# Kernel optimization log

Hardware: AMD Instinct MI355X
Metric: run time of the kernel (lower is better)

Reference implementation:

```python
import jax, jax.numpy as jnp
import numpy as np

# BiDiGemma (Aveygo/SRNext) wrapping RecurrentGemma-style ResidualBlocks:
#   block0 = RECURRENT (causal conv width 4 + RG-LRU linear recurrence)
#   block1 = local (sliding-window, MQA) ATTENTION with partial RoPE
# Dropout(0.1) is treated as eval-mode identity.

B, S, D, H = 4, 4096, 256, 4
HD = D // H            # head dim = 64
E = 3 * D              # mlp_expanded_width = expand_ratio * dim
W_ATT = D              # attention_window_size = dim = 256 (divides S)
TW = 4                 # recurrentgemma temporal conv width
_NEG = -2.3819763e38   # recurrentgemma masking constant

_PNAMES = ["ln_gamma","ln_beta","proj_w","proj_b","fconv_w","fconv_b","bconv_w","bconv_b",
 "rn0_t","rn0_c","ly_w","ly_b","lx_w","lx_b","lo_w","lo_b","c1d_w","c1d_b",
 "a_param","ig_w","ig_b","ag_w","ag_b","mlp0_up_w","mlp0_up_b","mlp0_dn_w","mlp0_dn_b",
 "rn1_t","rn1_c","q_w","k_w","v_w","o_w","o_b","mlp1_up_w","mlp1_up_b","mlp1_dn_w","mlp1_dn_b"]


def _init_params(key):
    ks = iter(jax.random.split(key, 24))
    nrm = lambda shape, s: jax.random.normal(next(ks), shape, jnp.float32) * s
    p = {}
    p["ln_gamma"] = jnp.ones((D,), jnp.float32); p["ln_beta"] = jnp.zeros((D,), jnp.float32)
    p["proj_w"] = nrm((D, D), D ** -0.5);  p["proj_b"] = jnp.zeros((D,), jnp.float32)
    p["fconv_w"] = nrm((D, D), D ** -0.5); p["fconv_b"] = jnp.zeros((D,), jnp.float32)
    p["bconv_w"] = nrm((D, D), D ** -0.5); p["bconv_b"] = jnp.zeros((D,), jnp.float32)
    p["rn0_t"] = jnp.zeros((D,), jnp.float32); p["rn0_c"] = jnp.zeros((D,), jnp.float32)
    p["ly_w"] = nrm((D, D), D ** -0.5); p["ly_b"] = jnp.zeros((D,), jnp.float32)
    p["lx_w"] = nrm((D, D), D ** -0.5); p["lx_b"] = jnp.zeros((D,), jnp.float32)
    p["lo_w"] = nrm((D, D), D ** -0.5); p["lo_b"] = jnp.zeros((D,), jnp.float32)
    p["c1d_w"] = nrm((TW, D), 0.1);     p["c1d_b"] = jnp.zeros((D,), jnp.float32)
    p["a_param"] = jnp.log(jnp.expm1(jnp.linspace(0.9, 1.5, D, dtype=jnp.float32)))
    p["ig_w"] = nrm((H, HD, HD), HD ** -0.5); p["ig_b"] = jnp.zeros((H, HD), jnp.float32)
    p["ag_w"] = nrm((H, HD, HD), HD ** -0.5); p["ag_b"] = jnp.zeros((H, HD), jnp.float32)
    p["mlp0_up_w"] = nrm((2, D, E), D ** -0.5); p["mlp0_up_b"] = jnp.zeros((2, E), jnp.float32)
    p["mlp0_dn_w"] = nrm((E, D), E ** -0.5);    p["mlp0_dn_b"] = jnp.zeros((D,), jnp.float32)
    p["rn1_t"] = jnp.zeros((D,), jnp.float32); p["rn1_c"] = jnp.zeros((D,), jnp.float32)
    p["q_w"] = nrm((D, D), D ** -0.5); p["k_w"] = nrm((D, HD), D ** -0.5); p["v_w"] = nrm((D, HD), D ** -0.5)
    p["o_w"] = nrm((D, D), D ** -0.5); p["o_b"] = jnp.zeros((D,), jnp.float32)
    p["mlp1_up_w"] = nrm((2, D, E), D ** -0.5); p["mlp1_up_b"] = jnp.zeros((2, E), jnp.float32)
    p["mlp1_dn_w"] = nrm((E, D), E ** -0.5);    p["mlp1_dn_b"] = jnp.zeros((D,), jnp.float32)
    return p


def _gelu(x):
    return jax.nn.gelu(x, approximate=False)  # torch F.gelu default (erf)


def _rms_norm(x, scale, eps=1e-6):
    var = jnp.mean(jnp.square(x), axis=-1, keepdims=True)
    return x * jax.lax.rsqrt(var + eps) * (1.0 + scale)


def _layer_norm(x, g, b, eps=1e-5):
    m = jnp.mean(x, axis=-1, keepdims=True)
    v = jnp.mean(jnp.square(x - m), axis=-1, keepdims=True)
    return (x - m) * jax.lax.rsqrt(v + eps) * g + b


def _block_diag(x, w, b):
    # BlockDiagonalLinear: per-head [HD x HD] blocks
    xh = x.reshape(*x.shape[:-1], H, HD)
    y = jnp.einsum('bshd,hdk->bshk', xh, w) + b
    return y.reshape(*x.shape)


def _causal_conv1d(x, w, b):
    # depthwise causal conv, w: [TW, D], w[TW-1] multiplies current token
    xp = jnp.pad(x, ((0, 0), (TW - 1, 0), (0, 0)))
    out = sum(xp[:, i:i + x.shape[1], :] * w[i] for i in range(TW))
    return out + b


def _rg_lru(x, pos, a_param, ig_w, ig_b, ag_w, ag_b):
    gate_x = jax.nn.sigmoid(_block_diag(x, ig_w, ig_b))
    gate_a = jax.nn.sigmoid(_block_diag(x, ag_w, ag_b))
    log_a = -8.0 * gate_a * jax.nn.softplus(a_param)   # c = 8
    a = jnp.exp(log_a)
    mult = jnp.sqrt(-jnp.expm1(2.0 * log_a))           # sqrt(1 - a^2)
    reset = (pos == 0)[..., None]
    mult = jnp.where(reset, 1.0, mult)
    bterm = x * gate_x * mult
    def comb(e1, e2):
        a1, b1 = e1
        a2, b2 = e2
        return a1 * a2, a2 * b1 + b2
    _, h = jax.lax.associative_scan(comb, (a, bterm), axis=1)
    return h


def _rope(x, pos):
    # partial RoPE: applied to first half of head dim (recurrentgemma)
    rot, rest = jnp.split(x, 2, axis=-1)
    f = rot.shape[-1] // 2
    inv_freq = 10000.0 ** (-(2.0 / rot.shape[-1]) * jnp.arange(f, dtype=jnp.float32))
    t = pos[..., None, None].astype(jnp.float32) * inv_freq  # [b, s, 1, f]
    sin, cos = jnp.sin(t), jnp.cos(t)
    x1, x2 = jnp.split(rot, 2, axis=-1)
    return jnp.concatenate([x1 * cos - x2 * sin, x2 * cos + x1 * sin, rest], axis=-1)


def _local_attention(x, pos, q_w, k_w, v_w, o_w, o_b):
    # MQA sliding-window attention, window = W_ATT; chunked to honor locality
    b, s, _ = x.shape
    q = (x @ q_w).reshape(b, s, H, HD)
    k = (x @ k_w).reshape(b, s, 1, HD)
    v = (x @ v_w).reshape(b, s, HD)
    q = _rope(q, pos) * (HD ** -0.5)
    k = _rope(k, pos)[:, :, 0]
    Wn = W_ATT
    nb = s // Wn
    qc = q.reshape(b, nb, Wn, H, HD)
    kp = jnp.pad(k, ((0, 0), (Wn, 0), (0, 0))).reshape(b, nb + 1, Wn, HD)
    vp = jnp.pad(v, ((0, 0), (Wn, 0), (0, 0))).reshape(b, nb + 1, Wn, HD)
    kc = jnp.concatenate([kp[:, :-1], kp[:, 1:]], axis=2)  # [b, nb, 2W, HD]
    vc = jnp.concatenate([vp[:, :-1], vp[:, 1:]], axis=2)
    logits = jnp.einsum('bnqhd,bnkd->bnhqk', qc, kc)
    i = jnp.arange(Wn)[:, None]
    j = jnp.arange(2 * Wn)[None, :]
    diff = (i + Wn) - j                       # q_pos - k_pos
    base = (diff >= 0) & (diff <= Wn)         # causal & q <= k + window_size
    cidx = jnp.arange(nb)[:, None, None]
    mask = base[None] & ((cidx > 0) | (j[None] >= Wn))  # no left padding in chunk 0
    logits = jnp.where(mask[None, :, None], logits, _NEG)
    probs = jax.nn.softmax(logits, axis=-1)
    out = jnp.einsum('bnhqk,bnkd->bnqhd', probs, vc).reshape(b, s, D)
    return out @ o_w + o_b


def _mlp(x, up_w, up_b, dn_w, dn_b):
    up = jnp.einsum('bsd,cde->cbse', x, up_w) + up_b[:, None, None, :]
    act = _gelu(up[0]) * up[1]
    return act @ dn_w + dn_b


def _gemma_block(x, pos, p):
    # ResidualBlock 0: RECURRENT
    raw = x
    xn = _rms_norm(raw, p['rn0_t'])
    y = _gelu(xn @ p['ly_w'] + p['ly_b'])
    xr = xn @ p['lx_w'] + p['lx_b']
    xr = _causal_conv1d(xr, p['c1d_w'], p['c1d_b'])
    xr = _rg_lru(xr, pos, p['a_param'], p['ig_w'], p['ig_b'], p['ag_w'], p['ag_b'])
    xr = (xr * y) @ p['lo_w'] + p['lo_b']
    residual = xr + raw
    x = _rms_norm(residual, p['rn0_c'])
    x = _mlp(x, p['mlp0_up_w'], p['mlp0_up_b'], p['mlp0_dn_w'], p['mlp0_dn_b']) + residual
    # ResidualBlock 1: local ATTENTION
    raw = x
    xn = _rms_norm(raw, p['rn1_t'])
    xa = _local_attention(xn, pos, p['q_w'], p['k_w'], p['v_w'], p['o_w'], p['o_b'])
    residual = xa + raw
    x = _rms_norm(residual, p['rn1_c'])
    x = _mlp(x, p['mlp1_up_w'], p['mlp1_up_b'], p['mlp1_dn_w'], p['mlp1_dn_b']) + residual
    return x


def _forward(skip, *params):
    p = dict(zip(_PNAMES, params))
    b, s, _ = skip.shape
    pos = jnp.broadcast_to(jnp.arange(s, dtype=jnp.int32)[None], (b, s))
    x = _layer_norm(skip, p['ln_gamma'], p['ln_beta']) @ p['proj_w'] + p['proj_b']
    z = jax.nn.sigmoid(jnp.mean(jax.nn.silu(skip), axis=-1, keepdims=True))
    fwd = _gemma_block(x @ p['fconv_w'] + p['fconv_b'], pos, p)  # Conv1d k=1 == pointwise
    bwd = _gemma_block(x @ p['bconv_w'] + p['bconv_b'], pos, p)
    return z * (fwd + bwd) + skip


def setup_inputs() -> dict:
    key = jax.random.key(0)
    kx, kp = jax.random.split(key)
    inp = {"skip": jax.random.normal(kx, (B, S, D), jnp.float32)}
    inp.update(_init_params(kp))
    return inp


def reference(skip, ln_gamma, ln_beta, proj_w, proj_b, fconv_w, fconv_b, bconv_w, bconv_b, rn0_t, rn0_c, ly_w, ly_b, lx_w, lx_b, lo_w, lo_b, c1d_w, c1d_b, a_param, ig_w, ig_b, ag_w, ag_b, mlp0_up_w, mlp0_up_b, mlp0_dn_w, mlp0_dn_b, rn1_t, rn1_c, q_w, k_w, v_w, o_w, o_b, mlp1_up_w, mlp1_up_b, mlp1_dn_w, mlp1_dn_b):
    return _forward(skip, ln_gamma, ln_beta, proj_w, proj_b, fconv_w, fconv_b, bconv_w, bconv_b, rn0_t, rn0_c, ly_w, ly_b, lx_w, lx_b, lo_w, lo_b, c1d_w, c1d_b, a_param, ig_w, ig_b, ag_w, ag_b, mlp0_up_w, mlp0_up_b, mlp0_dn_w, mlp0_dn_b, rn1_t, rn1_c, q_w, k_w, v_w, o_w, o_b, mlp1_up_w, mlp1_up_b, mlp1_dn_w, mlp1_dn_b)
```

## Files before the change

kernel.cpp:

```cpp
#include <hip/hip_runtime.h>
#include <math.h>
#include <stddef.h>


#define BB   4
#define SS   4096
#define DD   256
#define HH   4
#define HDIM 64
#define EE   768
#define RR   (BB*SS)
#define RR2  (2*RR)
#define WNN  256
#define CH   64
#define NCH  (SS/CH)

typedef __attribute__((ext_vector_type(8))) short bfrag;
typedef __attribute__((ext_vector_type(4))) float f4acc;

__device__ __forceinline__ float geluf(float x){
  float u = 1.5957691216f*(x + 0.044715f*x*x*x);
  float e = __expf(u);
  float t = 1.f - 2.f/(e+1.f);
  return 0.5f*x*(1.f+t);
}
__device__ __forceinline__ float sigm(float x){ return 1.0f/(1.0f+expf(-x)); }

__device__ __forceinline__ unsigned short f2bf(float x){
  unsigned u = __float_as_uint(x);
  return (unsigned short)((u + 0x7FFFu + ((u>>16)&1u)) >> 16);
}
__device__ __forceinline__ float bf2f(unsigned short h){
  return __uint_as_float(((unsigned)h) << 16);
}
__device__ __forceinline__ void split2(float v, unsigned short* h, unsigned short* l){
  unsigned short hb = f2bf(v);
  *h = hb; *l = f2bf(v - bf2f(hb));
}

__device__ __forceinline__ float wredSum(float v){
#pragma unroll
  for(int o=32;o>0;o>>=1) v += __shfl_xor(v,o,64);
  return v;
}

__global__ __launch_bounds__(256) void ln_z_k(const float* __restrict__ skip,
    const float* __restrict__ g, const float* __restrict__ b,
    unsigned short* __restrict__ oh, unsigned short* __restrict__ ol,
    float* __restrict__ z)
{
  int row  = blockIdx.x*4 + (threadIdx.x>>6);
  int lane = threadIdx.x & 63;
  float4 v = ((const float4*)(skip + (size_t)row*DD))[lane];
  float s  = v.x+v.y+v.z+v.w;
  float sq = v.x*v.x+v.y*v.y+v.z*v.z+v.w*v.w;
  float si = v.x*sigm(v.x)+v.y*sigm(v.y)+v.z*sigm(v.z)+v.w*sigm(v.w);
  s = wredSum(s); sq = wredSum(sq); si = wredSum(si);
  float mean = s*(1.0f/DD);
  float var  = sq*(1.0f/DD) - mean*mean;
  float inv  = rsqrtf(var + 1e-5f);
  float4 gv = ((const float4*)g)[lane];
  float4 bv = ((const float4*)b)[lane];
  float o0 = (v.x-mean)*inv*gv.x + bv.x;
  float o1 = (v.y-mean)*inv*gv.y + bv.y;
  float o2 = (v.z-mean)*inv*gv.z + bv.z;
  float o3 = (v.w-mean)*inv*gv.w + bv.w;
  ushort4 hi, lo;
  split2(o0,&hi.x,&lo.x); split2(o1,&hi.y,&lo.y);
  split2(o2,&hi.z,&lo.z); split2(o3,&hi.w,&lo.w);
  ((ushort4*)(oh + (size_t)row*DD))[lane] = hi;
  ((ushort4*)(ol + (size_t)row*DD))[lane] = lo;
  if(lane==0) z[row] = sigm(si*(1.0f/DD));
}

__global__ __launch_bounds__(256) void rms_k(const float* __restrict__ x,
    const float* __restrict__ t,
    unsigned short* __restrict__ oh, unsigned short* __restrict__ ol)
{
  int row  = blockIdx.x*4 + (threadIdx.x>>6);
  int lane = threadIdx.x & 63;
  float4 v = ((const float4*)(x + (size_t)row*DD))[lane];
  float sq = v.x*v.x+v.y*v.y+v.z*v.z+v.w*v.w;
  sq = wredSum(sq);
  float inv = rsqrtf(sq*(1.0f/DD) + 1e-6f);
  float4 tv = ((const float4*)t)[lane];
  float o0 = v.x*inv*(1.0f+tv.x);
  float o1 = v.y*inv*(1.0f+tv.y);
  float o2 = v.z*inv*(1.0f+tv.z);
  float o3 = v.w*inv*(1.0f+tv.w);
  ushort4 hi, lo;
  split2(o0,&hi.x,&lo.x); split2(o1,&hi.y,&lo.y);
  split2(o2,&hi.z,&lo.z); split2(o3,&hi.w,&lo.w);
  ((ushort4*)(oh + (size_t)row*DD))[lane] = hi;
  ((ushort4*)(ol + (size_t)row*DD))[lane] = lo;
}

struct TS  { const float* s; unsigned short* h; unsigned short* l; int K; int N; };
struct TS8 { TS t[8]; };

__global__ __launch_bounds__(256) void tsplit8_k(TS8 g){
  TS tt = g.t[blockIdx.y];
  int idx = blockIdx.x*256 + threadIdx.x;
  int tot = tt.K*tt.N;
  if(idx >= tot) return;
  int k = idx / tt.N;
  int n = idx - k*tt.N;
  float x = tt.s[idx];
  unsigned short hb = f2bf(x);
  unsigned short lb = f2bf(x - bf2f(hb));
  tt.h[(size_t)n*tt.K + k] = hb;
  tt.l[(size_t)n*tt.K + k] = lb;
}

template<int BN, int MODE, int DUAL, int OUT, int TERMS>
__global__ __launch_bounds__(256) void gemm_mfma(
    const unsigned short* __restrict__ Ah_g, const unsigned short* __restrict__ Al_g,
    const unsigned short* __restrict__ B0h, const unsigned short* __restrict__ B0l,
    const unsigned short* __restrict__ B1h, const unsigned short* __restrict__ B1l,
    const float* __restrict__ bias0, const float* __restrict__ bias1,
    const float* __restrict__ Res, float* __restrict__ C,
    unsigned short* __restrict__ Ch, unsigned short* __restrict__ Cl,
    int K, int lda, int ldc)
{
  constexpr int NT = BN/32;
  constexpr int ST = 40;
  __shared__ unsigned short Ash[128*ST];
  __shared__ unsigned short Asl[TERMS==3 ? 128*ST : 8];
  __shared__ unsigned short Bsh[BN*ST];
  __shared__ unsigned short Bsl[TERMS>=2 ? BN*ST : 8];
  __shared__ unsigned short B2h[DUAL?BN*ST:8];
  __shared__ unsigned short B2l[(DUAL && TERMS>=2)?BN*ST:8];

  const int tid  = threadIdx.x;
  const int lane = tid & 63, wave = tid >> 6;
  const int wm = wave >> 1, wn = wave & 1;
  const int bm = blockIdx.y*128, bn = blockIdx.x*BN;
  const int m16 = lane & 15, q = lane >> 4;

  f4acc acc[4][NT];
  f4acc acc2[DUAL?4:1][DUAL?NT:1];
#pragma unroll
  for(int i=0;i<4;i++)
#pragma unroll
    for(int j=0;j<NT;j++){
      acc[i][j] = (f4acc)0.f;
      if constexpr(DUAL) acc2[i][j] = (f4acc)0.f;
    }

  const int r0 = tid >> 2, c0 = tid & 3;
  const int coff = c0*8;
  const int d0 = r0*ST + coff, d1 = (r0+64)*ST + coff;

  const unsigned short* pAh0 = Ah_g + (size_t)(bm+r0)*lda + coff;
  const unsigned short* pAh1 = pAh0 + (size_t)64*lda;
  const unsigned short* pAl0 = (TERMS==3) ? (Al_g + (size_t)(bm+r0)*lda + coff)
                                          : (const unsigned short*)nullptr;
  const unsigned short* pAl1 = (TERMS==3) ? (pAl0 + (size_t)64*lda)
                                          : (const unsigned short*)nullptr;
  const unsigned short *pB0h0=nullptr,*pB0h1=nullptr,*pB0l0=nullptr,*pB0l1=nullptr;
  const unsigned short *pBa=nullptr,*pBb=nullptr,*pBc=nullptr,*pBd=nullptr;
  if constexpr(BN==128){
    pB0h0 = B0h + (size_t)(bn+r0)*K + coff;  pB0h1 = pB0h0 + (size_t)64*K;
    if constexpr(TERMS>=2){
      pB0l0 = B0l + (size_t)(bn+r0)*K + coff;  pB0l1 = pB0l0 + (size_t)64*K;
    }
  } else {
    pBa = B0h + (size_t)(bn+r0)*K + coff;
    if constexpr(TERMS>=2) pBb = B0l + (size_t)(bn+r0)*K + coff;
    if constexpr(DUAL){
      pBc = B1h + (size_t)(bn+r0)*K + coff;
      if constexpr(TERMS>=2) pBd = B1l + (size_t)(bn+r0)*K + coff;
    }
  }

  for(int k0 = 0; k0 < K; k0 += 32){
    *(float4*)&Ash[d0] = *(const float4*)(pAh0 + k0);
    *(float4*)&Ash[d1] = *(const float4*)(pAh1 + k0);
    if constexpr(TERMS==3){
      *(float4*)&Asl[d0] = *(const float4*)(pAl0 + k0);
      *(float4*)&Asl[d1] = *(const float4*)(pAl1 + k0);
    }
    if constexpr(BN==128){
      *(float4*)&Bsh[d0] = *(const float4*)(pB0h0 + k0);
      *(float4*)&Bsh[d1] = *(const float4*)(pB0h1 + k0);
      if constexpr(TERMS>=2){
        *(float4*)&Bsl[d0] = *(const float4*)(pB0l0 + k0);
        *(float4*)&Bsl[d1] = *(const float4*)(pB0l1 + k0);
      }
    } else {
      *(float4*)&Bsh[d0] = *(const float4*)(pBa + k0);
      if constexpr(TERMS>=2) *(float4*)&Bsl[d0] = *(const float4*)(pBb + k0);
      if constexpr(DUAL){
        *(float4*)&B2h[d0] = *(const float4*)(pBc + k0);
        if constexpr(TERMS>=2) *(float4*)&B2l[d0] = *(const float4*)(pBd + k0);
      }
    }
    __syncthreads();

    bfrag ah[4], al[TERMS==3?4:1], b0hf[NT], b0lf[TERMS>=2?NT:1];
    bfrag b1hf[DUAL?NT:1], b1lf[(DUAL&&TERMS>=2)?NT:1];
#pragma unroll
    for(int mi=0;mi<4;mi++){
      int row = wm*64 + mi*16 + m16;
      ah[mi] = *(const bfrag*)&Ash[row*ST + q*8];
      if constexpr(TERMS==3) al[mi] = *(const bfrag*)&Asl[row*ST + q*8];
    }
#pragma unroll
    for(int ni=0;ni<NT;ni++){
      int n = wn*(BN/2) + ni*16 + m16;
      b0hf[ni] = *(const bfrag*)&Bsh[n*ST + q*8];
      if constexpr(TERMS>=2) b0lf[ni] = *(const bfrag*)&Bsl[n*ST + q*8];
      if constexpr(DUAL){
        b1hf[ni] = *(const bfrag*)&B2h[n*ST + q*8];
        if constexpr(TERMS>=2) b1lf[ni] = *(const bfrag*)&B2l[n*ST + q*8];
      }
    }
#pragma unroll
    for(int mi=0;mi<4;mi++)
#pragma unroll
      for(int ni=0;ni<NT;ni++){
        acc[mi][ni] = __builtin_amdgcn_mfma_f32_16x16x32_bf16(ah[mi], b0hf[ni], acc[mi][ni],0,0,0);
        if constexpr(TERMS>=2)
          acc[mi][ni] = __builtin_amdgcn_mfma_f32_16x16x32_bf16(ah[mi], b0lf[ni], acc[mi][ni],0,0,0);
        if constexpr(TERMS==3)
          acc[mi][ni] = __builtin_amdgcn_mfma_f32_16x16x32_bf16(al[mi], b0hf[ni], acc[mi][ni],0,0,0);
        if constexpr(DUAL){
          acc2[mi][ni] = __builtin_amdgcn_mfma_f32_16x16x32_bf16(ah[mi], b1hf[ni], acc2[mi][ni],0,0,0);
          if constexpr(TERMS>=2)
            acc2[mi][ni] = __builtin_amdgcn_mfma_f32_16x16x32_bf16(ah[mi], b1lf[ni], acc2[mi][ni],0,0,0);
          if constexpr(TERMS==3)
            acc2[mi][ni] = __builtin_amdgcn_mfma_f32_16x16x32_bf16(al[mi], b1hf[ni], acc2[mi][ni],0,0,0);
        }
      }
    __syncthreads();
  }

  if constexpr(OUT==0 || OUT==1 || OUT==5){
#pragma unroll
    for(int ni=0;ni<NT;ni++){
      const int col = bn + wn*(BN/2) + ni*16 + m16;
      float bv0 = (MODE&1) ? bias0[col] : 0.f;
      float bv1 = DUAL ? bias1[col] : 0.f;
#pragma unroll
      for(int mi=0;mi<4;mi++){
#pragma unroll
        for(int r=0;r<4;r++){
          const int row = bm + wm*64 + mi*16 + q*4 + r;
          float v = acc[mi][ni][r] + bv0;
          if constexpr(DUAL){
            float v2 = acc2[mi][ni][r] + bv1;
            v = geluf(v) * v2;
          } else if(MODE&2){
            v = geluf(v);
          }
          if(MODE&8) v += Res[(size_t)row*ldc + col];
          if constexpr(OUT==0){
            C[(size_t)row*ldc + col] = v;
          } else if constexpr(OUT==1){
            unsigned short hb = f2bf(v);
            Ch[(size_t)row*ldc + col] = hb;
            Cl[(size_t)row*ldc + col] = f2bf(v - bf2f(hb));
          } else {
            Ch[(size_t)row*ldc + col] = f2bf(v);
          }
        }
      }
    }
  } else if constexpr(OUT==2){
    const int hb = bn + wn*64;
    const float p = (float)m16;
    const float invf = __expf(-p * 0.575646273248511f);
#pragma unroll
    for(int mi=0;mi<4;mi++){
#pragma unroll
      for(int r=0;r<4;r++){
        const int row = bm + wm*64 + mi*16 + q*4 + r;
        const int s = row & (SS-1);
        float t = (float)s * invf;
        float sn, cs; __sincosf(t, &sn, &cs);
        float x1 = acc[mi][0][r], x2 = acc[mi][1][r];
        float v0 = (x1*cs - x2*sn)*0.125f;
        float v1 = (x2*cs + x1*sn)*0.125f;
        float v2 = acc[mi][2][r]*0.125f;
        float v3 = acc[mi][3][r]*0.125f;
        size_t base = (size_t)row*ldc + hb;
        unsigned short hh;
        hh=f2bf(v0); Ch[base+m16]=hh;    Cl[base+m16]   =f2bf(v0-bf2f(hh));
        hh=f2bf(v1); Ch[base+16+m16]=hh; Cl[base+16+m16]=f2bf(v1-bf2f(hh));
        hh=f2bf(v2); Ch[base+32+m16]=hh; Cl[base+32+m16]=f2bf(v2-bf2f(hh));
        hh=f2bf(v3); Ch[base+48+m16]=hh; Cl[base+48+m16]=f2bf(v3-bf2f(hh));
      }
    }
  } else if constexpr(OUT==3){
    const float p = (float)m16;
    const float invf = __expf(-p * 0.575646273248511f);
#pragma unroll
    for(int mi=0;mi<4;mi++){
#pragma unroll
      for(int r=0;r<4;r++){
        const int row = bm + wm*64 + mi*16 + q*4 + r;
        const int s = row & (SS-1);
        float v0, v1;
        if(wn==0){
          float t = (float)s * invf;
          float sn, cs; __sincosf(t, &sn, &cs);
          float x1 = acc[mi][0][r], x2 = acc[mi][1][r];
          v0 = x1*cs - x2*sn;
          v1 = x2*cs + x1*sn;
        } else {
          v0 = acc[mi][0][r]; v1 = acc[mi][1][r];
        }
        size_t base = (size_t)row*ldc + wn*32;
        unsigned short hh;
        hh=f2bf(v0); Ch[base+m16]=hh;    Cl[base+m16]   =f2bf(v0-bf2f(hh));
        hh=f2bf(v1); Ch[base+16+m16]=hh; Cl[base+16+m16]=f2bf(v1-bf2f(hh));
      }
    }
  } else if constexpr(OUT==4){
#pragma unroll
    for(int ni=0;ni<NT;ni++){
      const int col = wn*32 + ni*16 + m16;
#pragma unroll
      for(int mi=0;mi<4;mi++){
        const int rowb = bm + wm*64 + mi*16 + q*4;
        const int b = rowb >> 12, sl = rowb & (SS-1);
        ushort4 hv;
        hv.x = f2bf(acc[mi][ni][0]); hv.y = f2bf(acc[mi][ni][1]);
        hv.z = f2bf(acc[mi][ni][2]); hv.w = f2bf(acc[mi][ni][3]);
        *(ushort4*)(Ch + ((size_t)(b*64 + col))*SS + sl) = hv;
      }
    }
  }
}

__global__ __launch_bounds__(256) void conv_split_k(const float* __restrict__ x,
    const float* __restrict__ w, const float* __restrict__ b,
    unsigned short* __restrict__ oh, unsigned short* __restrict__ ol)
{
  int idx = blockIdx.x*256 + threadIdx.x;
  int d = idx & (DD-1);
  int r = idx >> 8;
  int s = r & (SS-1);
  float acc = b[d];
#pragma unroll
  for(int i=0;i<4;i++){
    int t = s - 3 + i;
    if(t >= 0) acc += w[i*DD + d] * x[(size_t)(r-3+i)*DD + d];
  }
  unsigned short hb = f2bf(acc);
  oh[idx] = hb;
  ol[idx] = f2bf(acc - bf2f(hb));
}

__global__ __launch_bounds__(256) void gates_mfma_k(
    const unsigned short* __restrict__ Xh, const unsigned short* __restrict__ Xl,
    const unsigned short* __restrict__ igth, const unsigned short* __restrict__ igtl,
    const unsigned short* __restrict__ agth, const unsigned short* __restrict__ agtl,
    const float* __restrict__ igb, const float* __restrict__ agb,
    const float* __restrict__ ap,
    float* __restrict__ Aout, float* __restrict__ Bout)
{
  constexpr int ST = 72;
  __shared__ unsigned short Ash[128*ST];
  __shared__ unsigned short Asl[128*ST];

  const int h  = blockIdx.x;
  const int bm = blockIdx.y*128;
  const int tid = threadIdx.x;
  const int lane = tid & 63, wave = tid >> 6;
  const int wm = wave >> 1, wn = wave & 1;
  const int m16 = lane & 15, q = lane >> 4;

  {
    const int r = tid >> 1, kq = (tid & 1)*32;
    const size_t src = (size_t)(bm + r)*DD + h*HDIM + kq;
    const int dst = r*ST + kq;
#pragma unroll
    for(int i=0;i<4;i++){
      *(float4*)&Ash[dst + i*8] = *(const float4*)(Xh + src + i*8);
      *(float4*)&Asl[dst + i*8] = *(const float4*)(Xl + src + i*8);
    }
  }
  __syncthreads();

  f4acc accI[4][2], accA[4][2];
#pragma unroll
  for(int i=0;i<4;i++)
#pragma unroll
    for(int j=0;j<2;j++){ accI[i][j]=(f4acc)0.f; accA[i][j]=(f4acc)0.f; }

  const size_t wbase = (size_t)h*HDIM*HDIM;
#pragma unroll
  for(int ks=0;ks<2;ks++){
    bfrag ah[4], al[4];
#pragma unroll
    for(int mi=0;mi<4;mi++){
      const int row = wm*64 + mi*16 + m16;
      ah[mi] = *(const bfrag*)&Ash[row*ST + ks*32 + q*8];
      al[mi] = *(const bfrag*)&Asl[row*ST + ks*32 + q*8];
    }
#pragma unroll
    for(int ni=0;ni<2;ni++){
      const size_t bo = wbase + (size_t)(wn*32 + ni*16 + m16)*HDIM + ks*32 + q*8;
      bfrag bIh = *(const bfrag*)(igth + bo);
      bfrag bIl = *(const bfrag*)(igtl + bo);
      bfrag bAh = *(const bfrag*)(agth + bo);
      bfrag bAl = *(const bfrag*)(agtl + bo);
#pragma unroll
      for(int mi=0;mi<4;mi++){
        accI[mi][ni] = __builtin_amdgcn_mfma_f32_16x16x32_bf16(ah[mi], bIh, accI[mi][ni],0,0,0);
        accI[mi][ni] = __builtin_amdgcn_mfma_f32_16x16x32_bf16(ah[mi], bIl, accI[mi][ni],0,0,0);
        accI[mi][ni] = __builtin_amdgcn_mfma_f32_16x16x32_bf16(al[mi], bIh, accI[mi][ni],0,0,0);
        accA[mi][ni] = __builtin_amdgcn_mfma_f32_16x16x32_bf16(ah[mi], bAh, accA[mi][ni],0,0,0);
        accA[mi][ni] = __builtin_amdgcn_mfma_f32_16x16x32_bf16(ah[mi], bAl, accA[mi][ni],0,0,0);
        accA[mi][ni] = __builtin_amdgcn_mfma_f32_16x16x32_bf16(al[mi], bAh, accA[mi][ni],0,0,0);
      }
    }
  }

#pragma unroll
  for(int ni=0;ni<2;ni++){
    const int cl  = wn*32 + ni*16 + m16;
    const int col = h*HDIM + cl;
    const float bI = igb[col], bA = agb[col];
    const float apv = ap[col];
    const float sp = (apv > 20.f) ? apv : log1pf(expf(apv));
#pragma unroll
    for(int mi=0;mi<4;mi++){
#pragma unroll
      for(int r=0;r<4;r++){
        const int lrow = wm*64 + mi*16 + q*4 + r;
        const int row = bm + lrow;
        const int s = row & (SS-1);
        float gx = 1.f/(1.f + __expf(-(accI[mi][ni][r] + bI)));
        float ga = 1.f/(1.f + __expf(-(accA[mi][ni][r] + bA)));
        float la = -8.f * ga * sp;
        float a_ = __expf(la);
        float mult = (s==0) ? 1.f : sqrtf(fmaxf(1.f - __expf(2.f*la), 0.f));
        float x = bf2f(Ash[lrow*ST + cl]) + bf2f(Asl[lrow*ST + cl]);
        Aout[(size_t)row*DD + col] = a_;
        Bout[(size_t)row*DD + col] = x * gx * mult;
      }
    }
  }
}

__global__ __launch_bounds__(256) void scan1_k(const float* __restrict__ A,
    const float* __restrict__ Bv, float* __restrict__ csa, float* __restrict__ csb)
{
  int idx = blockIdx.x*256 + threadIdx.x;
  int d = idx & (DD-1);
  int c = (idx >> 8) & (NCH-1);
  int b = idx >> 14;
  size_t base = ((size_t)b*SS + (size_t)c*CH)*DD + d;
  float Aa = 1.f, Bb_ = 0.f;
  for(int t=0;t<CH;t++){
    float a  = A [base + (size_t)t*DD];
    float bb = Bv[base + (size_t)t*DD];
    Aa  = a*Aa;
    Bb_ = a*Bb_ + bb;
  }
  csa[idx] = Aa; csb[idx] = Bb_;
}

__global__ __launch_bounds__(256) void scan2_k(const float* __restrict__ csa,
    float* __restrict__ csb)
{
  int idx = blockIdx.x*256 + threadIdx.x;
  int d = idx & (DD-1);
  int b = idx >> 8;
  float h = 0.f;
  for(int c=0;c<NCH;c++){
    size_t i = ((size_t)b*NCH + c)*DD + d;
    float Aa = csa[i], Bb_ = csb[i];
    csb[i] = h;
    h = Aa*h + Bb_;
  }
}

__global__ __launch_bounds__(256) void scan3_k(const float* __restrict__ A,
    const float* __restrict__ Bv, const float* __restrict__ csb,
    const unsigned short* __restrict__ Yh,
    unsigned short* __restrict__ Hh, unsigned short* __restrict__ Hl)
{
  int idx = blockIdx.x*256 + threadIdx.x;
  int d = idx & (DD-1);
  int c = (idx >> 8) & (NCH-1);
  int b = idx >> 14;
  size_t base = ((size_t)b*SS + (size_t)c*CH)*DD + d;
  float h = csb[idx];
  for(int t=0;t<CH;t++){
    float a  = A [base + (size_t)t*DD];
    float bb = Bv[base + (size_t)t*DD];
    h = a*h + bb;
    float v = h * bf2f(Yh[base + (size_t)t*DD]);
    unsigned short hb = f2bf(v);
    Hh[base + (size_t)t*DD] = hb;
    Hl[base + (size_t)t*DD] = f2bf(v - bf2f(hb));
  }
}

#define AST 72
__global__ __launch_bounds__(256) void attn_k(
    const unsigned short* __restrict__ Qh, const unsigned short* __restrict__ Ql,
    const unsigned short* __restrict__ Kh, const unsigned short* __restrict__ Kl,
    const unsigned short* __restrict__ Vt,
    unsigned short* __restrict__ Oh, unsigned short* __restrict__ Ol)
{
  __shared__ unsigned short Ksh[64*AST], Ksl[64*AST], Vsh[64*AST];
  __shared__ unsigned short Ps[4*16*AST];

  const int qt = blockIdx.x & 3, n = blockIdx.x >> 2;
  const int h = blockIdx.y, b = blockIdx.z;
  const int tid = threadIdx.x;
  const int lane = tid & 63, w = tid >> 6;
  const int m16 = lane & 15, q = lane >> 4;
  const int s0 = n*WNN + qt*64;

  const size_t qro = ((size_t)(b*SS + s0 + w*16 + m16))*DD + h*HDIM + q*8;
  bfrag qh0 = *(const bfrag*)(Qh + qro);
  bfrag qh1 = *(const bfrag*)(Qh + qro + 32);
  bfrag ql0 = *(const bfrag*)(Ql + qro);
  bfrag ql1 = *(const bfrag*)(Ql + qro + 32);

  float mrow[4], lrow[4];
  f4acc oacc[4];
#pragma unroll
  for(int i=0;i<4;i++){ mrow[i]=-3.0e38f; lrow[i]=0.f; oacc[i]=(f4acc)0.f; }

  const int ktlo = (n==0) ? 4 : qt;
  const int kthi = qt + 4;
  const int sr = tid >> 2, sc = tid & 3;

  for(int kt=ktlo; kt<=kthi; kt++){
    const int kbase = (n-1)*WNN + kt*64;
#pragma unroll
    for(int cc=0; cc<2; cc++){
      int g = sc + cc*4;
      *(float4*)&Ksh[sr*AST + g*8] =
        *(const float4*)(Kh + (size_t)(b*SS + kbase + sr)*HDIM + g*8);
      *(float4*)&Ksl[sr*AST + g*8] =
        *(const float4*)(Kl + (size_t)(b*SS + kbase + sr)*HDIM + g*8);
      *(float4*)&Vsh[sr*AST + g*8] =
        *(const float4*)(Vt + ((size_t)(b*64 + sr))*SS + kbase + g*8);
    }
    __syncthreads();

    f4acc sacc[4];
#pragma unroll
    for(int nt=0;nt<4;nt++) sacc[nt] = (f4acc)0.f;
#pragma unroll
    for(int nt=0;nt<4;nt++){
      const int kr = (nt*16+m16)*AST;
      bfrag kh0 = *(const bfrag*)&Ksh[kr + q*8];
      bfrag kh1 = *(const bfrag*)&Ksh[kr + 32 + q*8];
      bfrag kl0 = *(const bfrag*)&Ksl[kr + q*8];
      bfrag kl1 = *(const bfrag*)&Ksl[kr + 32 + q*8];
      sacc[nt] = __builtin_amdgcn_mfma_f32_16x16x32_bf16(qh0, kh0, sacc[nt],0,0,0);
      sacc[nt] = __builtin_amdgcn_mfma_f32_16x16x32_bf16(qh0, kl0, sacc[nt],0,0,0);
      sacc[nt] = __builtin_amdgcn_mfma_f32_16x16x32_bf16(ql0, kh0, sacc[nt],0,0,0);
      sacc[nt] = __builtin_amdgcn_mfma_f32_16x16x32_bf16(qh1, kh1, sacc[nt],0,0,0);
      sacc[nt] = __builtin_amdgcn_mfma_f32_16x16x32_bf16(qh1, kl1, sacc[nt],0,0,0);
      sacc[nt] = __builtin_amdgcn_mfma_f32_16x16x32_bf16(ql1, kh1, sacc[nt],0,0,0);
    }

    const bool needlo = (kt == qt+4);
    const bool needhi = (kt == qt);
#pragma unroll
    for(int r=0;r<4;r++){
      int qp = qt*64 + w*16 + q*4 + r;
      float sv[4];
      float tm = -3.0e38f;
#pragma unroll
      for(int nt=0;nt<4;nt++){
        float scv = sacc[nt][r];
        if(needlo || needhi){
          int kj = kt*64 + nt*16 + m16;
          int diff = qp + WNN - kj;
          bool ok = (!needlo || diff >= 0) && (!needhi || diff <= WNN);
          scv = ok ? scv : -3.0e38f;
        }
        sv[nt] = scv;
        tm = fmaxf(tm, scv);
      }
#pragma unroll
      for(int off=1; off<16; off<<=1) tm = fmaxf(tm, __shfl_xor(tm, off, 64));
      float mn = fmaxf(mrow[r], tm);
      float alpha = __expf(mrow[r]-mn);
      float rs = 0.f;
#pragma unroll
      for(int nt=0;nt<4;nt++){
        float pp = __expf(sv[nt]-mn);
        rs += pp;
        Ps[w*16*AST + (q*4+r)*AST + nt*16 + m16] = f2bf(pp);
      }
#pragma unroll
      for(int off=1; off<16; off<<=1) rs += __shfl_xor(rs, off, 64);
      lrow[r] = lrow[r]*alpha + rs;
      mrow[r] = mn;
#pragma unroll
      for(int nt=0;nt<4;nt++) oacc[nt][r] *= alpha;
    }

#pragma unroll
    for(int s=0;s<2;s++){
      bfrag pa = *(const bfrag*)&Ps[w*16*AST + m16*AST + s*32 + q*8];
#pragma unroll
      for(int nt=0;nt<4;nt++){
        bfrag vh_ = *(const bfrag*)&Vsh[(nt*16+m16)*AST + s*32 + q*8];
        oacc[nt] = __builtin_amdgcn_mfma_f32_16x16x32_bf16(pa, vh_, oacc[nt],0,0,0);
      }
    }
    __syncthreads();
  }

#pragma unroll
  for(int r=0;r<4;r++){
    float invl = 1.f/lrow[r];
    const size_t rowbase = ((size_t)(b*SS + s0 + w*16 + q*4 + r))*DD + h*HDIM;
#pragma unroll
    for(int nt=0;nt<4;nt++){
      float v = oacc[nt][r]*invl;
      unsigned short hb = f2bf(v);
      Oh[rowbase + nt*16 + m16] = hb;
      Ol[rowbase + nt*16 + m16] = f2bf(v - bf2f(hb));
    }
  }
}

__global__ __launch_bounds__(256) void comb_k(const float* __restrict__ of,
    const float* __restrict__ ob, const float* __restrict__ z,
    const float* __restrict__ skip, float* __restrict__ out)
{
  int idx = blockIdx.x*256 + threadIdx.x;
  int r = idx >> 8;
  out[idx] = z[r]*(of[idx]+ob[idx]) + skip[idx];
}

struct Params {
  const float *ln_gamma,*ln_beta,*proj_w,*proj_b,*fconv_w,*fconv_b,*bconv_w,*bconv_b,
    *rn0_t,*rn0_c,*ly_w,*ly_b,*lx_w,*lx_b,*lo_w,*lo_b,*c1d_w,*c1d_b,*a_param,
    *ig_w,*ig_b,*ag_w,*ag_b,*mlp0_up_w,*mlp0_up_b,*mlp0_dn_w,*mlp0_dn_b,
    *rn1_t,*rn1_c,*q_w,*k_w,*v_w,*o_w,*o_b,*mlp1_up_w,*mlp1_up_b,*mlp1_dn_w,*mlp1_dn_b;
};

struct WSplit {
  unsigned short *proj_h,*proj_l,*fconv_h,*fconv_l,*bconv_h,*bconv_l,
    *ly_h,*ly_l,*lx_h,*lx_l,*lo_h,*lo_l,*q_h,*q_l,*o_h,*o_l,
    *k_h,*k_l,*v_h,*v_l,
    *up0a_h,*up0a_l,*up0b_h,*up0b_l,*up1a_h,*up1a_l,*up1b_h,*up1b_l,
    *dn0_h,*dn0_l,*dn1_h,*dn1_l,
    *igt_h,*igt_l,*agt_h,*agt_l;
};

#define USN ((unsigned short*)nullptr)

extern "C" void kernel_launch(void* const* d_in, const int* in_sizes, int n_in,
                              void* d_out, int out_size, void* d_ws, size_t ws_size,
                              hipStream_t stream)
{
  (void)in_sizes; (void)n_in; (void)out_size; (void)ws_size;
  const float* skip = (const float*)d_in[0];
  Params p;
  p.ln_gamma  =(const float*)d_in[1];  p.ln_beta  =(const float*)d_in[2];
  p.proj_w    =(const float*)d_in[3];  p.proj_b   =(const float*)d_in[4];
  p.fconv_w   =(const float*)d_in[5];  p.fconv_b  =(const float*)d_in[6];
  p.bconv_w   =(const float*)d_in[7];  p.bconv_b  =(const float*)d_in[8];
  p.rn0_t     =(const float*)d_in[9];  p.rn0_c    =(const float*)d_in[10];
  p.ly_w      =(const float*)d_in[11]; p.ly_b     =(const float*)d_in[12];
  p.lx_w      =(const float*)d_in[13]; p.lx_b     =(const float*)d_in[14];
  p.lo_w      =(const float*)d_in[15]; p.lo_b     =(const float*)d_in[16];
  p.c1d_w     =(const float*)d_in[17]; p.c1d_b    =(const float*)d_in[18];
  p.a_param   =(const float*)d_in[19];
  p.ig_w      =(const float*)d_in[20]; p.ig_b     =(const float*)d_in[21];
  p.ag_w      =(const float*)d_in[22]; p.ag_b     =(const float*)d_in[23];
  p.mlp0_up_w =(const float*)d_in[24]; p.mlp0_up_b=(const float*)d_in[25];
  p.mlp0_dn_w =(const float*)d_in[26]; p.mlp0_dn_b=(const float*)d_in[27];
  p.rn1_t     =(const float*)d_in[28]; p.rn1_c    =(const float*)d_in[29];
  p.q_w       =(const float*)d_in[30]; p.k_w      =(const float*)d_in[31];
  p.v_w       =(const float*)d_in[32]; p.o_w      =(const float*)d_in[33];
  p.o_b       =(const float*)d_in[34];
  p.mlp1_up_w =(const float*)d_in[35]; p.mlp1_up_b=(const float*)d_in[36];
  p.mlp1_dn_w =(const float*)d_in[37]; p.mlp1_dn_b=(const float*)d_in[38];

  float* ws = (float*)d_ws;
  const size_t RD  = (size_t)RR*DD;
  const size_t PD2 = (size_t)RR2*DD;
  size_t off = 0;
  float* Z   = ws + off; off += 16384;
  float* XB2 = ws + off; off += 2*RD;
  float* CV2 = ws + off; off += 2*RD;
  float* W1  = ws + off; off += 2*RD;
  float* W2  = ws + off; off += 2*RD;
  float* W3  = ws + off; off += RD;
  float* W4  = ws + off; off += 2*RD;

  float* CSA = CV2;
  float* CSB = CV2 + 8*NCH*DD;

  unsigned short* NPh = (unsigned short*)W4;  unsigned short* NPl = NPh + PD2;
  unsigned short* HYh = NPh;                  unsigned short* HYl = NPl;
  unsigned short* CVh = NPh;                  unsigned short* CVl = NPl;
  unsigned short* X0h = (unsigned short*)W1;  unsigned short* X0l = X0h + (size_t)RR*DD;
  float* XR2 = W1;
  unsigned short* Qph = (unsigned short*)W1;  unsigned short* Qpl = Qph + PD2;
  float* Abuf = W2;
  unsigned short* P2h = (unsigned short*)W2;  unsigned short* P2l = P2h + PD2;
  unsigned short* Yh  = (unsigned short*)W3;
  unsigned short* KPh = (unsigned short*)W3;  unsigned short* KPl = KPh + (size_t)RR2*HDIM;
  unsigned short* Vt  = KPl + (size_t)RR2*HDIM;
  unsigned short* ACTh = (unsigned short*)W1;
  float* OUT2 = XB2;

  unsigned short* sp = (unsigned short*)(ws + off);
  WSplit w;
  auto alloc_s = [&](size_t n){ unsigned short* r = sp; sp += n; return r; };
  const size_t SDD = (size_t)DD*DD, SKV = (size_t)DD*HDIM, SUP = (size_t)DD*EE;
  const size_t SBD = (size_t)HH*HDIM*HDIM;
  w.proj_h=alloc_s(SDD);  w.proj_l=alloc_s(SDD);
  w.fconv_h=alloc_s(SDD); w.fconv_l=alloc_s(SDD);
  w.bconv_h=alloc_s(SDD); w.bconv_l=alloc_s(SDD);
  w.ly_h=alloc_s(SDD);    w.ly_l=alloc_s(SDD);
  w.lx_h=alloc_s(SDD);    w.lx_l=alloc_s(SDD);
  w.lo_h=alloc_s(SDD);    w.lo_l=alloc_s(SDD);
  w.q_h=alloc_s(SDD);     w.q_l=alloc_s(SDD);
  w.o_h=alloc_s(SDD);     w.o_l=alloc_s(SDD);
  w.k_h=alloc_s(SKV);     w.k_l=alloc_s(SKV);
  w.v_h=alloc_s(SKV);     w.v_l=alloc_s(SKV);
  w.up0a_h=alloc_s(SUP);  w.up0a_l=alloc_s(SUP);
  w.up0b_h=alloc_s(SUP);  w.up0b_l=alloc_s(SUP);
  w.up1a_h=alloc_s(SUP);  w.up1a_l=alloc_s(SUP);
  w.up1b_h=alloc_s(SUP);  w.up1b_l=alloc_s(SUP);
  w.dn0_h=alloc_s(SUP);   w.dn0_l=alloc_s(SUP);
  w.dn1_h=alloc_s(SUP);   w.dn1_l=alloc_s(SUP);
  w.igt_h=alloc_s(SBD);   w.igt_l=alloc_s(SBD);
  w.agt_h=alloc_s(SBD);   w.agt_l=alloc_s(SBD);

  dim3 blk(256);
  dim3 g2(2,128,1);
  dim3 g2m(2,256,1), g64m(1,256,1), gdual(12,256,1);
  dim3 ggm(HH, RR2/128, 1);

  {
    TS8 ga;
    ga.t[0] = {p.proj_w,  w.proj_h,  w.proj_l,  DD, DD};
    ga.t[1] = {p.fconv_w, w.fconv_h, w.fconv_l, DD, DD};
    ga.t[2] = {p.bconv_w, w.bconv_h, w.bconv_l, DD, DD};
    ga.t[3] = {p.ly_w,    w.ly_h,    w.ly_l,    DD, DD};
    ga.t[4] = {p.lx_w,    w.lx_h,    w.lx_l,    DD, DD};
    ga.t[5] = {p.lo_w,    w.lo_h,    w.lo_l,    DD, DD};
    ga.t[6] = {p.q_w,     w.q_h,     w.q_l,     DD, DD};
    ga.t[7] = {p.o_w,     w.o_h,     w.o_l,     DD, DD};
    tsplit8_k<<<dim3(DD*DD/256, 8), blk, 0, stream>>>(ga);
    TS8 gb;
    gb.t[0] = {p.k_w,              w.k_h,    w.k_l,    DD, HDIM};
    gb.t[1] = {p.v_w,              w.v_h,    w.v_l,    DD, HDIM};
    gb.t[2] = {p.mlp0_up_w,        w.up0a_h, w.up0a_l, DD, EE};
    gb.t[3] = {p.mlp0_up_w+(size_t)DD*EE, w.up0b_h, w.up0b_l, DD, EE};
    gb.t[4] = {p.mlp1_up_w,        w.up1a_h, w.up1a_l, DD, EE};
    gb.t[5] = {p.mlp1_up_w+(size_t)DD*EE, w.up1b_h, w.up1b_l, DD, EE};
    gb.t[6] = {p.mlp0_dn_w,        w.dn0_h,  w.dn0_l,  EE, DD};
    gb.t[7] = {p.mlp1_dn_w,        w.dn1_h,  w.dn1_l,  EE, DD};
    tsplit8_k<<<dim3(DD*EE/256, 8), blk, 0, stream>>>(gb);
    TS8 gc;
    for(int h=0;h<HH;h++){
      gc.t[h]   = {p.ig_w + (size_t)h*HDIM*HDIM, w.igt_h + (size_t)h*HDIM*HDIM,
                   w.igt_l + (size_t)h*HDIM*HDIM, HDIM, HDIM};
      gc.t[4+h] = {p.ag_w + (size_t)h*HDIM*HDIM, w.agt_h + (size_t)h*HDIM*HDIM,
                   w.agt_l + (size_t)h*HDIM*HDIM, HDIM, HDIM};
    }
    tsplit8_k<<<dim3(HDIM*HDIM/256, 8), blk, 0, stream>>>(gc);
  }

  ln_z_k<<<RR/4, blk, 0, stream>>>(skip, p.ln_gamma, p.ln_beta, NPh, NPl, Z);
  gemm_mfma<128,1,0,1,3><<<g2,blk,0,stream>>>(NPh,NPl, w.proj_h,w.proj_l, USN,USN,
      p.proj_b,nullptr,nullptr, nullptr, X0h, X0l, DD,DD,DD);
  gemm_mfma<128,1,0,0,3><<<g2,blk,0,stream>>>(X0h,X0l, w.fconv_h,w.fconv_l, USN,USN,
      p.fconv_b,nullptr,nullptr, XB2, USN,USN, DD,DD,DD);
  gemm_mfma<128,1,0,0,3><<<g2,blk,0,stream>>>(X0h,X0l, w.bconv_h,w.bconv_l, USN,USN,
      p.bconv_b,nullptr,nullptr, XB2 + RD, USN,USN, DD,DD,DD);

  rms_k<<<RR2/4, blk, 0, stream>>>(XB2, p.rn0_t, NPh, NPl);
  gemm_mfma<128,3,0,5,2><<<g2m,blk,0,stream>>>(NPh,USN, w.ly_h,w.ly_l, USN,USN,
      p.ly_b,nullptr,nullptr, nullptr, Yh, USN, DD,DD,DD);
  gemm_mfma<128,1,0,0,2><<<g2m,blk,0,stream>>>(NPh,USN, w.lx_h,w.lx_l, USN,USN,
      p.lx_b,nullptr,nullptr, XR2, USN,USN, DD,DD,DD);
  conv_split_k<<<(size_t)RR2*DD/256, blk, 0, stream>>>(XR2, p.c1d_w, p.c1d_b, CVh, CVl);
  gates_mfma_k<<<ggm,blk,0,stream>>>(CVh, CVl, w.igt_h, w.igt_l, w.agt_h, w.agt_l,
      p.ig_b, p.ag_b, p.a_param, Abuf, XR2);
  scan1_k<<<8*NCH*DD/256, blk,0,stream>>>(Abuf, XR2, CSA, CSB);
  scan2_k<<<8*DD/256, blk,0,stream>>>(CSA, CSB);
  scan3_k<<<8*NCH*DD/256, blk,0,stream>>>(Abuf, XR2, CSB, Yh, HYh, HYl);
  gemm_mfma<128,9,0,0,2><<<g2m,blk,0,stream>>>(HYh,USN, w.lo_h,w.lo_l, USN,USN,
      p.lo_b,nullptr, XB2, CV2, USN,USN, DD,DD,DD);
  rms_k<<<RR2/4,blk,0,stream>>>(CV2, p.rn0_c, NPh, NPl);
  gemm_mfma<64,1,1,5,1><<<gdual,blk,0,stream>>>(NPh,USN, w.up0a_h,USN,
      w.up0b_h,USN, p.mlp0_up_b, p.mlp0_up_b+EE, nullptr, nullptr,
      ACTh, USN, DD,DD,EE);
  gemm_mfma<128,9,0,0,2><<<g2m,blk,0,stream>>>(ACTh,USN, w.dn0_h,w.dn0_l, USN,USN,
      p.mlp0_dn_b,nullptr, CV2, XB2, USN,USN, EE,EE,DD);

  rms_k<<<RR2/4,blk,0,stream>>>(XB2, p.rn1_t, NPh, NPl);
  gemm_mfma<128,0,0,2,2><<<g2m,blk,0,stream>>>(NPh,USN, w.q_h,w.q_l, USN,USN,
      nullptr,nullptr,nullptr, nullptr, Qph, Qpl, DD,DD,DD);
  gemm_mfma<64,0,0,3,3><<<g64m,blk,0,stream>>>(NPh,NPl, w.k_h,w.k_l, USN,USN,
      nullptr,nullptr,nullptr, nullptr, KPh, KPl, DD,DD,HDIM);
  gemm_mfma<64,0,0,4,3><<<g64m,blk,0,stream>>>(NPh,NPl, w.v_h,w.v_l, USN,USN,
      nullptr,nullptr,nullptr, nullptr, Vt, USN, DD,DD,HDIM);
  attn_k<<<dim3(64,4,8),blk,0,stream>>>(Qph, Qpl, KPh, KPl, Vt, P2h, P2l);
  gemm_mfma<128,9,0,0,2><<<g2m,blk,0,stream>>>(P2h,USN, w.o_h,w.o_l, USN,USN,
      p.o_b,nullptr, XB2, CV2, USN,USN, DD,DD,DD);
  rms_k<<<RR2/4,blk,0,stream>>>(CV2, p.rn1_c, NPh, NPl);
  gemm_mfma<64,1,1,5,1><<<gdual,blk,0,stream>>>(NPh,USN, w.up1a_h,USN,
      w.up1b_h,USN, p.mlp1_up_b, p.mlp1_up_b+EE, nullptr, nullptr,
      ACTh, USN, DD,DD,EE);
  gemm_mfma<128,9,0,0,2><<<g2m,blk,0,stream>>>(ACTh,USN, w.dn1_h,w.dn1_l, USN,USN,
      p.mlp1_dn_b,nullptr, CV2, OUT2, USN,USN, EE,EE,DD);

  comb_k<<<RR*DD/256, blk, 0, stream>>>(OUT2, OUT2 + RD, Z, skip, (float*)d_out);
}
```

Before: 752.5 us.

## Fuse causal conv into gates kernel, merge K/V GEMMs, drop low-split scan output

Folds the width-4 causal conv into the gates MFMA kernel's shared-memory load, removing the separate conv_split_k pass and its hi/lo bf16 intermediate buffers. The K and V projections are combined into one dual-output GEMM with a new epilogue (OUT==7) that applies RoPE to K and writes V transposed, saving one launch and one read of the normed input. scan3 now writes only the high bf16 part, since the following GEMM ignores the low part. The gates output B goes to a separate buffer. The fused conv recomputes a few halo rows per strip, and the new epilogue must reproduce the earlier K RoPE and V layout exactly.

```diff
diff --git a/kernel.cpp b/kernel.cpp
--- a/kernel.cpp
+++ b/kernel.cpp
@@ -330,30 +330,53 @@
         *(ushort4*)(Ch + ((size_t)(b*64 + col))*SS + sl) = hv;
       }
     }
-  }
-}
-
-__global__ __launch_bounds__(256) void conv_split_k(const float* __restrict__ x,
-    const float* __restrict__ w, const float* __restrict__ b,
-    unsigned short* __restrict__ oh, unsigned short* __restrict__ ol)
-{
-  int idx = blockIdx.x*256 + threadIdx.x;
-  int d = idx & (DD-1);
-  int r = idx >> 8;
-  int s = r & (SS-1);
-  float acc = b[d];
-#pragma unroll
-  for(int i=0;i<4;i++){
-    int t = s - 3 + i;
-    if(t >= 0) acc += w[i*DD + d] * x[(size_t)(r-3+i)*DD + d];
-  }
-  unsigned short hb = f2bf(acc);
-  oh[idx] = hb;
-  ol[idx] = f2bf(acc - bf2f(hb));
-}
-
-__global__ __launch_bounds__(256) void gates_mfma_k(
-    const unsigned short* __restrict__ Xh, const unsigned short* __restrict__ Xl,
+  } else if constexpr(OUT==7){
+    const float p = (float)m16;
+    const float invf = __expf(-p * 0.575646273248511f);
+#pragma unroll
+    for(int mi=0;mi<4;mi++){
+#pragma unroll
+      for(int r=0;r<4;r++){
+        const int row = bm + wm*64 + mi*16 + q*4 + r;
+        const int s = row & (SS-1);
+        float v0, v1;
+        if(wn==0){
+          float t = (float)s * invf;
+          float sn, cs; __sincosf(t, &sn, &cs);
+          float x1 = acc[mi][0][r], x2 = acc[mi][1][r];
+          v0 = x1*cs - x2*sn;
+          v1 = x2*cs + x1*sn;
+        } else {
+          v0 = acc[mi][0][r]; v1 = acc[mi][1][r];
+        }
+        size_t base = (size_t)row*ldc + wn*32;
+        unsigned short hh;
+        hh=f2bf(v0); Ch[base+m16]=hh;    Cl[base+m16]   =f2bf(v0-bf2f(hh));
+        hh=f2bf(v1); Ch[base+16+m16]=hh; Cl[base+16+m16]=f2bf(v1-bf2f(hh));
+      }
+    }
+    if constexpr(DUAL){
+      unsigned short* Cv = (unsigned short*)C;
+#pragma unroll
+      for(int ni=0;ni<NT;ni++){
+        const int col = wn*32 + ni*16 + m16;
+#pragma unroll
+        for(int mi=0;mi<4;mi++){
+          const int rowb = bm + wm*64 + mi*16 + q*4;
+          const int b = rowb >> 12, sl = rowb & (SS-1);
+          ushort4 hv;
+          hv.x = f2bf(acc2[mi][ni][0]); hv.y = f2bf(acc2[mi][ni][1]);
+          hv.z = f2bf(acc2[mi][ni][2]); hv.w = f2bf(acc2[mi][ni][3]);
+          *(ushort4*)(Cv + ((size_t)(b*64 + col))*SS + sl) = hv;
+        }
+      }
+    }
+  }
+}
+
+__global__ __launch_bounds__(256) void gates_conv_k(
+    const float* __restrict__ X,
+    const float* __restrict__ cw, const float* __restrict__ cb,
     const unsigned short* __restrict__ igth, const unsigned short* __restrict__ igtl,
     const unsigned short* __restrict__ agth, const unsigned short* __restrict__ agtl,
     const float* __restrict__ igb, const float* __restrict__ agb,
@@ -372,13 +395,49 @@
   const int m16 = lane & 15, q = lane >> 4;
 
   {
-    const int r = tid >> 1, kq = (tid & 1)*32;
-    const size_t src = (size_t)(bm + r)*DD + h*HDIM + kq;
-    const int dst = r*ST + kq;
-#pragma unroll
-    for(int i=0;i<4;i++){
-      *(float4*)&Ash[dst + i*8] = *(const float4*)(Xh + src + i*8);
-      *(float4*)&Asl[dst + i*8] = *(const float4*)(Xl + src + i*8);
+    const int strip = tid >> 4;
+    const int cg = (tid & 15)*4;
+    const int col0 = h*HDIM + cg;
+    const int r0 = bm + strip*8;
+    float h0[4], h1[4], h2[4];
+#pragma unroll
+    for(int i=0;i<3;i++){
+      int rr = r0 - 3 + i;
+      int rc = rr < 0 ? 0 : rr;
+      float4 hv = *(const float4*)(X + (size_t)rc*DD + col0);
+      float* dst = (i==0)?h0:((i==1)?h1:h2);
+      dst[0]=hv.x; dst[1]=hv.y; dst[2]=hv.z; dst[3]=hv.w;
+    }
+    float4 w0v = *(const float4*)(cw + 0*DD + col0);
+    float4 w1v = *(const float4*)(cw + 1*DD + col0);
+    float4 w2v = *(const float4*)(cw + 2*DD + col0);
+    float4 w3v = *(const float4*)(cw + 3*DD + col0);
+    float4 bbv = *(const float4*)(cb + col0);
+    const float* w0 = (const float*)&w0v; const float* w1 = (const float*)&w1v;
+    const float* w2 = (const float*)&w2v; const float* w3 = (const float*)&w3v;
+    const float* bb = (const float*)&bbv;
+    for(int rr=0; rr<8; rr++){
+      const int r = r0 + rr;
+      const int s = r & (SS-1);
+      float4 cv = *(const float4*)(X + (size_t)r*DD + col0);
+      float cur[4]; cur[0]=cv.x; cur[1]=cv.y; cur[2]=cv.z; cur[3]=cv.w;
+      ushort4 hi, lo;
+      unsigned short* hp = (unsigned short*)&hi;
+      unsigned short* lp = (unsigned short*)&lo;
+#pragma unroll
+      for(int j=0;j<4;j++){
+        float acc = bb[j] + w3[j]*cur[j];
+        if(s>=1) acc += w2[j]*h2[j];
+        if(s>=2) acc += w1[j]*h1[j];
+        if(s>=3) acc += w0[j]*h0[j];
+        unsigned short hb = f2bf(acc);
+        hp[j] = hb; lp[j] = f2bf(acc - bf2f(hb));
+      }
+      const int dst = (strip*8+rr)*ST + cg;
+      *(ushort4*)&Ash[dst] = hi;
+      *(ushort4*)&Asl[dst] = lo;
+#pragma unroll
+      for(int j=0;j<4;j++){ h0[j]=h1[j]; h1[j]=h2[j]; h2[j]=cur[j]; }
     }
   }
   __syncthreads();
@@ -481,7 +540,7 @@
 __global__ __launch_bounds__(256) void scan3_k(const float* __restrict__ A,
     const float* __restrict__ Bv, const float* __restrict__ csb,
     const unsigned short* __restrict__ Yh,
-    unsigned short* __restrict__ Hh, unsigned short* __restrict__ Hl)
+    unsigned short* __restrict__ Hh)
 {
   int idx = blockIdx.x*256 + threadIdx.x;
   int d = idx & (DD-1);
@@ -494,9 +553,7 @@
     float bb = Bv[base + (size_t)t*DD];
     h = a*h + bb;
     float v = h * bf2f(Yh[base + (size_t)t*DD]);
-    unsigned short hb = f2bf(v);
-    Hh[base + (size_t)t*DD] = hb;
-    Hl[base + (size_t)t*DD] = f2bf(v - bf2f(hb));
+    Hh[base + (size_t)t*DD] = f2bf(v);
   }
 }
 
@@ -699,8 +756,8 @@
   float* CSB = CV2 + 8*NCH*DD;
 
   unsigned short* NPh = (unsigned short*)W4;  unsigned short* NPl = NPh + PD2;
-  unsigned short* HYh = NPh;                  unsigned short* HYl = NPl;
-  unsigned short* CVh = NPh;                  unsigned short* CVl = NPl;
+  float* BT = W4;
+  unsigned short* HYh = (unsigned short*)W1;
   unsigned short* X0h = (unsigned short*)W1;  unsigned short* X0l = X0h + (size_t)RR*DD;
   float* XR2 = W1;
   unsigned short* Qph = (unsigned short*)W1;  unsigned short* Qpl = Qph + PD2;
@@ -785,12 +842,11 @@
       p.ly_b,nullptr,nullptr, nullptr, Yh, USN, DD,DD,DD);
   gemm_mfma<128,1,0,0,2><<<g2m,blk,0,stream>>>(NPh,USN, w.lx_h,w.lx_l, USN,USN,
       p.lx_b,nullptr,nullptr, XR2, USN,USN, DD,DD,DD);
-  conv_split_k<<<(size_t)RR2*DD/256, blk, 0, stream>>>(XR2, p.c1d_w, p.c1d_b, CVh, CVl);
-  gates_mfma_k<<<ggm,blk,0,stream>>>(CVh, CVl, w.igt_h, w.igt_l, w.agt_h, w.agt_l,
-      p.ig_b, p.ag_b, p.a_param, Abuf, XR2);
-  scan1_k<<<8*NCH*DD/256, blk,0,stream>>>(Abuf, XR2, CSA, CSB);
+  gates_conv_k<<<ggm,blk,0,stream>>>(XR2, p.c1d_w, p.c1d_b,
+      w.igt_h, w.igt_l, w.agt_h, w.agt_l, p.ig_b, p.ag_b, p.a_param, Abuf, BT);
+  scan1_k<<<8*NCH*DD/256, blk,0,stream>>>(Abuf, BT, CSA, CSB);
   scan2_k<<<8*DD/256, blk,0,stream>>>(CSA, CSB);
-  scan3_k<<<8*NCH*DD/256, blk,0,stream>>>(Abuf, XR2, CSB, Yh, HYh, HYl);
+  scan3_k<<<8*NCH*DD/256, blk,0,stream>>>(Abuf, BT, CSB, Yh, HYh);
   gemm_mfma<128,9,0,0,2><<<g2m,blk,0,stream>>>(HYh,USN, w.lo_h,w.lo_l, USN,USN,
       p.lo_b,nullptr, XB2, CV2, USN,USN, DD,DD,DD);
   rms_k<<<RR2/4,blk,0,stream>>>(CV2, p.rn0_c, NPh, NPl);
@@ -803,10 +859,8 @@
   rms_k<<<RR2/4,blk,0,stream>>>(XB2, p.rn1_t, NPh, NPl);
   gemm_mfma<128,0,0,2,2><<<g2m,blk,0,stream>>>(NPh,USN, w.q_h,w.q_l, USN,USN,
       nullptr,nullptr,nullptr, nullptr, Qph, Qpl, DD,DD,DD);
-  gemm_mfma<64,0,0,3,3><<<g64m,blk,0,stream>>>(NPh,NPl, w.k_h,w.k_l, USN,USN,
-      nullptr,nullptr,nullptr, nullptr, KPh, KPl, DD,DD,HDIM);
-  gemm_mfma<64,0,0,4,3><<<g64m,blk,0,stream>>>(NPh,NPl, w.v_h,w.v_l, USN,USN,
-      nullptr,nullptr,nullptr, nullptr, Vt, USN, DD,DD,HDIM);
+  gemm_mfma<64,0,1,7,3><<<g64m,blk,0,stream>>>(NPh,NPl, w.k_h,w.k_l, w.v_h,w.v_l,
+      nullptr,nullptr,nullptr, (float*)Vt, KPh, KPl, DD,DD,HDIM);
   attn_k<<<dim3(64,4,8),blk,0,stream>>>(Qph, Qpl, KPh, KPl, Vt, P2h, P2l);
   gemm_mfma<128,9,0,0,2><<<g2m,blk,0,stream>>>(P2h,USN, w.o_h,w.o_l, USN,USN,
       p.o_b,nullptr, XB2, CV2, USN,USN, DD,DD,DD);
```

Result: faster. 712.4 us (-5.3%).
